# Kernel tuning notes

Measured on AMD Instinct MI355X. Metric: run time of the kernel, lower is better.

## Reference

```python
import jax, jax.numpy as jnp
import numpy as np

N = 100000
E = 3200000
IN_CH = 512
H1 = 16


def setup_inputs() -> dict:
    key = jax.random.key(0)
    ks = jax.random.split(key, 9)
    x = jax.random.normal(ks[0], (N, IN_CH), dtype=jnp.float32)
    edge_index = jax.random.randint(ks[1], (2, E), 0, N, dtype=jnp.int64)
    # GCNConv params: weight [in, out], bias [out]
    def glorot(k, fan_in, fan_out):
        lim = (6.0 / (fan_in + fan_out)) ** 0.5
        return jax.random.uniform(k, (fan_in, fan_out), jnp.float32, -lim, lim)
    W1 = glorot(ks[2], IN_CH, H1)
    b1 = jnp.zeros((H1,), jnp.float32)
    W2 = glorot(ks[3], H1, H1)
    b2 = jnp.zeros((H1,), jnp.float32)
    W3 = glorot(ks[4], H1, 1)
    b3 = jnp.zeros((1,), jnp.float32)
    return {"x": x, "edge_index": edge_index, "W1": W1, "b1": b1,
            "W2": W2, "b2": b2, "W3": W3, "b3": b3}


def _gcn_conv(x, W, b, src, dst, deg_isqrt):
    # GCNConv: h = X W; out = D^-1/2 (A + I) D^-1/2 h + b
    h = x @ W  # [N, out]
    norm = deg_isqrt[src] * deg_isqrt[dst]  # [E]
    msg = h[src] * norm[:, None]  # gather + scale
    agg = jax.ops.segment_sum(msg, dst, num_segments=N)  # scatter-add
    agg = agg + h * (deg_isqrt * deg_isqrt)[:, None]  # self-loop term
    return agg + b


def reference(x, edge_index, W1, b1, W2, b2, W3, b3):
    src, dst = edge_index[0], edge_index[1]
    # degree of A + I, counted on destination nodes (symmetric norm)
    deg = jax.ops.segment_sum(jnp.ones((E,), jnp.float32), dst, num_segments=N) + 1.0
    deg_isqrt = jax.lax.rsqrt(deg)
    h = _gcn_conv(x, W1, b1, src, dst, deg_isqrt)
    h = jax.nn.relu(h)  # dropout is identity at eval
    h = _gcn_conv(h, W2, b2, src, dst, deg_isqrt)
    h = jax.nn.relu(h)
    out = _gcn_conv(h, W3, b3, src, dst, deg_isqrt)
    return out
```

## Files before the change

kernel.cpp:

```cpp
#include <hip/hip_runtime.h>
#include <hip/hip_bf16.h>

static constexpr int N_NODES = 100000;
static constexpr int N_EDGES = 3200000;
static constexpr int IN_CH = 512;
static constexpr int H = 16;
static constexpr int TB = 256;

static constexpr int BN = 256;
static constexpr int NB = (N_NODES + BN - 1) / BN;
static constexpr int CAP = 8960;
static constexpr int CAP2 = CAP + 3 * BN;
static constexpr int CHUNK = 8192;
static constexpr int GRID_SC = (N_EDGES + CHUNK - 1) / CHUNK;
static constexpr int NBLK64 = (N_NODES + 63) / 64;

__global__ void k_init(int* __restrict__ gcur) {
  int b = blockIdx.x * blockDim.x + threadIdx.x;
  if (b < NB) gcur[b] = b * CAP;
}

__global__ void k_cscatter(const int* __restrict__ ei, int* __restrict__ gcur,
                           int* __restrict__ ebuf) {
  __shared__ int cnt[NB];
  __shared__ int gofs[NB];
  int t = threadIdx.x;
  int c0 = blockIdx.x * CHUNK;
  int c1 = min(c0 + CHUNK, N_EDGES);
  for (int b = t; b < NB; b += TB) cnt[b] = 0;
  __syncthreads();
  for (int j = c0 + t; j < c1; j += TB) atomicAdd(&cnt[ei[N_EDGES + j] >> 8], 1);
  __syncthreads();
  for (int b = t; b < NB; b += TB)
    if (cnt[b] > 0) gofs[b] = atomicAdd(&gcur[b], cnt[b]);
  __syncthreads();
  for (int j = c0 + t; j < c1; j += TB) {
    int s = ei[j];
    int d = ei[N_EDGES + j];
    int slot = atomicAdd(&gofs[d >> 8], 1);
    ebuf[slot] = ((d & 255) << 17) | s;
  }
}

__global__ void k_bsort(const int* __restrict__ gcur, const int* __restrict__ ebuf,
                        int* __restrict__ ebuf2, int* __restrict__ nrs,
                        int* __restrict__ nend, float* __restrict__ disq) {
  __shared__ int cnt[BN];
  __shared__ int pre[BN];
  __shared__ int cur[BN];
  int b = blockIdx.x, t = threadIdx.x;
  cnt[t] = 0;
  __syncthreads();
  int beg = b * CAP, end = gcur[b];
  for (int j = beg + t; j < end; j += TB) atomicAdd(&cnt[ebuf[j] >> 17], 1);
  __syncthreads();
  int myc = cnt[t];
  int ac = (myc + 3) & ~3;
  pre[t] = ac;
  __syncthreads();
  for (int off = 1; off < TB; off <<= 1) {
    int v = (t >= off) ? pre[t - off] : 0;
    __syncthreads();
    pre[t] += v;
    __syncthreads();
  }
  int start = b * CAP2 + ((t == 0) ? 0 : pre[t - 1]);
  cur[t] = start;
  int node = b * BN + t;
  if (node < N_NODES) {
    nrs[node] = start;
    nend[node] = start + ac;
    disq[node] = 1.0f / sqrtf((float)myc + 1.0f);
    for (int j = start + myc; j < start + ac; j++) ebuf2[j] = N_NODES;
  }
  __syncthreads();
  for (int j = beg + t; j < end; j += TB) {
    int p = ebuf[j];
    int slot = atomicAdd(&cur[p >> 17], 1);
    ebuf2[slot] = p & 0x1FFFF;
  }
}

__global__ void k_gemm1(const float* __restrict__ x, const float* __restrict__ W,
                        const float* __restrict__ disq,
                        float* __restrict__ hloA, float* __restrict__ hhiA,
                        float* __restrict__ hloB, float* __restrict__ hhiB,
                        float* __restrict__ hs3) {
  int r = blockIdx.x * blockDim.x + threadIdx.x;
  if (r > N_NODES) return;
  if (r == N_NODES) {
    float4 z = make_float4(0.f, 0.f, 0.f, 0.f);
    ((float4*)(hloA + (size_t)r * 8))[0] = z;
    ((float4*)(hloA + (size_t)r * 8))[1] = z;
    ((float4*)(hhiA + (size_t)r * 8))[0] = z;
    ((float4*)(hhiA + (size_t)r * 8))[1] = z;
    ((float4*)(hloB + (size_t)r * 8))[0] = z;
    ((float4*)(hloB + (size_t)r * 8))[1] = z;
    ((float4*)(hhiB + (size_t)r * 8))[0] = z;
    ((float4*)(hhiB + (size_t)r * 8))[1] = z;
    hs3[r] = 0.f;
    return;
  }
  const float4* xr = (const float4*)(x + (size_t)r * IN_CH);
  float acc[H];
#pragma unroll
  for (int c = 0; c < H; c++) acc[c] = 0.f;
  for (int k4 = 0; k4 < IN_CH / 4; k4++) {
    float4 xv = xr[k4];
    const float* wr = W + k4 * 4 * H;
    float xs[4] = {xv.x, xv.y, xv.z, xv.w};
#pragma unroll
    for (int j = 0; j < 4; j++) {
#pragma unroll
      for (int c = 0; c < H; c++) acc[c] = fmaf(xs[j], wr[j * H + c], acc[c]);
    }
  }
  float dn = disq[r];
  float4* lo = (float4*)(hloA + (size_t)r * 8);
  float4* hi = (float4*)(hhiA + (size_t)r * 8);
  lo[0] = make_float4(acc[0] * dn, acc[1] * dn, acc[2] * dn, acc[3] * dn);
  lo[1] = make_float4(acc[4] * dn, acc[5] * dn, acc[6] * dn, acc[7] * dn);
  hi[0] = make_float4(acc[8] * dn, acc[9] * dn, acc[10] * dn, acc[11] * dn);
  hi[1] = make_float4(acc[12] * dn, acc[13] * dn, acc[14] * dn, acc[15] * dn);
}

__global__ void k_gath_mid(const int* __restrict__ nrs, const int* __restrict__ nend,
                           const int* __restrict__ ebuf2, const float* __restrict__ disq,
                           const float* __restrict__ inlo, const float* __restrict__ inhi,
                           const float* __restrict__ W2, const float* __restrict__ bias,
                           float* __restrict__ outlo, float* __restrict__ outhi) {
  __shared__ float agg[64 * 16];
  __shared__ float w[256];
  int b = blockIdx.x, t = threadIdx.x;
  w[t] = W2[t];
  int grp = t >> 3, lane = t & 7;
#pragma unroll
  for (int ph = 0; ph < 2; ph++) {
    const float* hs = ph ? inhi : inlo;
#pragma unroll
    for (int k = 0; k < 2; k++) {
      int node = b * 64 + grp * 2 + k;
      if (node < N_NODES) {
        int beg = nrs[node], endp = nend[node];
        float acc = 0.f;
        for (int j = beg; j < endp; j += 4) {
          int4 s = *(const int4*)(ebuf2 + j);
          float a0 = hs[(size_t)s.x * 8 + lane];
          float a1 = hs[(size_t)s.y * 8 + lane];
          float a2 = hs[(size_t)s.z * 8 + lane];
          float a3 = hs[(size_t)s.w * 8 + lane];
          acc += (a0 + a1) + (a2 + a3);
        }
        float dn = disq[node];
        agg[(grp * 2 + k) * 16 + ph * 8 + lane] =
            fmaf(acc + hs[(size_t)node * 8 + lane], dn, bias[ph * 8 + lane]);
      }
    }
  }
  __syncthreads();
  int nl = t >> 2, q = t & 3;
  int node = b * 64 + nl;
  if (node < N_NODES) {
    float o0 = 0.f, o1 = 0.f, o2 = 0.f, o3 = 0.f;
#pragma unroll
    for (int c4 = 0; c4 < 4; c4++) {
      float4 av = *(const float4*)(agg + nl * 16 + c4 * 4);
      float vs[4] = {av.x, av.y, av.z, av.w};
#pragma unroll
      for (int i2 = 0; i2 < 4; i2++) {
        float v = fmaxf(vs[i2], 0.f);
        const float* wr = w + (c4 * 4 + i2) * 16 + q * 4;
        o0 = fmaf(v, wr[0], o0);
        o1 = fmaf(v, wr[1], o1);
        o2 = fmaf(v, wr[2], o2);
        o3 = fmaf(v, wr[3], o3);
      }
    }
    float dn = disq[node];
    float4 r = make_float4(o0 * dn, o1 * dn, o2 * dn, o3 * dn);
    if (q < 2) *(float4*)(outlo + (size_t)node * 8 + q * 4) = r;
    else *(float4*)(outhi + (size_t)node * 8 + (q - 2) * 4) = r;
  }
}

__global__ void k_gath_last(const int* __restrict__ nrs, const int* __restrict__ nend,
                            const int* __restrict__ ebuf2, const float* __restrict__ disq,
                            const float* __restrict__ inlo, const float* __restrict__ inhi,
                            const float* __restrict__ W3, const float* __restrict__ bias,
                            float* __restrict__ hs3) {
  __shared__ float agg[64 * 16];
  __shared__ float w3[16];
  int b = blockIdx.x, t = threadIdx.x;
  if (t < 16) w3[t] = W3[t];
  int grp = t >> 3, lane = t & 7;
#pragma unroll
  for (int ph = 0; ph < 2; ph++) {
    const float* hs = ph ? inhi : inlo;
#pragma unroll
    for (int k = 0; k < 2; k++) {
      int node = b * 64 + grp * 2 + k;
      if (node < N_NODES) {
        int beg = nrs[node], endp = nend[node];
        float acc = 0.f;
        for (int j = beg; j < endp; j += 4) {
          int4 s = *(const int4*)(ebuf2 + j);
          float a0 = hs[(size_t)s.x * 8 + lane];
          float a1 = hs[(size_t)s.y * 8 + lane];
          float a2 = hs[(size_t)s.z * 8 + lane];
          float a3 = hs[(size_t)s.w * 8 + lane];
          acc += (a0 + a1) + (a2 + a3);
        }
        float dn = disq[node];
        agg[(grp * 2 + k) * 16 + ph * 8 + lane] =
            fmaf(acc + hs[(size_t)node * 8 + lane], dn, bias[ph * 8 + lane]);
      }
    }
  }
  __syncthreads();
  int nl = t >> 2, q = t & 3;
  int node = b * 64 + nl;
  if (node < N_NODES) {
    float4 av = *(const float4*)(agg + nl * 16 + q * 4);
    float o = fmaxf(av.x, 0.f) * w3[q * 4 + 0];
    o = fmaf(fmaxf(av.y, 0.f), w3[q * 4 + 1], o);
    o = fmaf(fmaxf(av.z, 0.f), w3[q * 4 + 2], o);
    o = fmaf(fmaxf(av.w, 0.f), w3[q * 4 + 3], o);
    o += __shfl_xor(o, 1);
    o += __shfl_xor(o, 2);
    if (q == 0) hs3[node] = o * disq[node];
  }
}

__global__ void k_gath1(const int* __restrict__ nrs, const int* __restrict__ nend,
                        const int* __restrict__ ebuf2, const float* __restrict__ disq,
                        const float* __restrict__ hs3, const float* __restrict__ bias,
                        float* __restrict__ out) {
  int b = blockIdx.x, t = threadIdx.x;
  int nl = t >> 2, lane = t & 3;
  int node = b * 64 + nl;
  if (node >= N_NODES) return;
  int beg = nrs[node], endp = nend[node];
  float acc = 0.f;
  for (int j = beg + 4 * lane; j < endp; j += 16) {
    int4 s = *(const int4*)(ebuf2 + j);
    acc += (hs3[s.x] + hs3[s.y]) + (hs3[s.z] + hs3[s.w]);
  }
  acc += __shfl_xor(acc, 1);
  acc += __shfl_xor(acc, 2);
  if (lane == 0) out[node] = fmaf(acc + hs3[node], disq[node], bias[0]);
}

extern "C" void kernel_launch(void* const* d_in, const int* in_sizes, int n_in,
                              void* d_out, int out_size, void* d_ws, size_t ws_size,
                              hipStream_t stream) {
  const float* x = (const float*)d_in[0];
  const int* ei = (const int*)d_in[1];
  const float* W1 = (const float*)d_in[2];
  const float* b1 = (const float*)d_in[3];
  const float* W2 = (const float*)d_in[4];
  const float* b2 = (const float*)d_in[5];
  const float* W3 = (const float*)d_in[6];
  const float* b3 = (const float*)d_in[7];
  float* out = (float*)d_out;

  int* ebuf = (int*)d_ws;
  int* ebuf2 = ebuf + (size_t)NB * CAP;
  int* gcur = ebuf2 + (size_t)NB * CAP2;
  int* nrs = gcur + NB;
  int* nend = nrs + N_NODES;
  int pad = (4 - ((NB + 2 * N_NODES) & 3)) & 3;
  float* disq = (float*)(nend + N_NODES + pad);
  float* hloA = disq + N_NODES;
  float* hhiA = hloA + (size_t)(N_NODES + 1) * 8;
  float* hloB = hhiA + (size_t)(N_NODES + 1) * 8;
  float* hhiB = hloB + (size_t)(N_NODES + 1) * 8;
  float* hs3 = hhiB + (size_t)(N_NODES + 1) * 8;

  k_init<<<(NB + 63) / 64, 64, 0, stream>>>(gcur);
  k_cscatter<<<GRID_SC, TB, 0, stream>>>(ei, gcur, ebuf);
  k_bsort<<<NB, TB, 0, stream>>>(gcur, ebuf, ebuf2, nrs, nend, disq);

  k_gemm1<<<(N_NODES + 64) / 64, 64, 0, stream>>>(x, W1, disq, hloA, hhiA, hloB, hhiB, hs3);
  k_gath_mid<<<NBLK64, TB, 0, stream>>>(nrs, nend, ebuf2, disq, hloA, hhiA, W2, b1, hloB, hhiB);
  k_gath_last<<<NBLK64, TB, 0, stream>>>(nrs, nend, ebuf2, disq, hloB, hhiB, W3, b2, hs3);
  k_gath1<<<NBLK64, TB, 0, stream>>>(nrs, nend, ebuf2, disq, hs3, b3, out);
}
```

Measured before the change: 552.4 us.

## Store hidden features as contiguous 16-float rows and gather with float4 loads

Replaces the split lo/hi 8-float feature buffers with one 64-byte row per node. The gather kernels now use 4 lanes per node, each loading a float4, instead of 8 lanes doing scalar loads over two passes. The last layer's gather and W3 projection are fused into registers, which drops the shared-memory staging and a block sync. The aim is fewer, wider memory transactions per edge and fewer passes over the edge list, with one 64-byte line per neighbour instead of two 32-byte segments. In exchange each thread holds more loads in flight, and there are fewer threads per node.

```diff
diff --git a/kernel.cpp b/kernel.cpp
--- a/kernel.cpp
+++ b/kernel.cpp
@@ -83,21 +83,17 @@
 
 __global__ void k_gemm1(const float* __restrict__ x, const float* __restrict__ W,
                         const float* __restrict__ disq,
-                        float* __restrict__ hloA, float* __restrict__ hhiA,
-                        float* __restrict__ hloB, float* __restrict__ hhiB,
+                        float* __restrict__ hsA, float* __restrict__ hsB,
                         float* __restrict__ hs3) {
   int r = blockIdx.x * blockDim.x + threadIdx.x;
   if (r > N_NODES) return;
   if (r == N_NODES) {
     float4 z = make_float4(0.f, 0.f, 0.f, 0.f);
-    ((float4*)(hloA + (size_t)r * 8))[0] = z;
-    ((float4*)(hloA + (size_t)r * 8))[1] = z;
-    ((float4*)(hhiA + (size_t)r * 8))[0] = z;
-    ((float4*)(hhiA + (size_t)r * 8))[1] = z;
-    ((float4*)(hloB + (size_t)r * 8))[0] = z;
-    ((float4*)(hloB + (size_t)r * 8))[1] = z;
-    ((float4*)(hhiB + (size_t)r * 8))[0] = z;
-    ((float4*)(hhiB + (size_t)r * 8))[1] = z;
+#pragma unroll
+    for (int q = 0; q < 4; q++) {
+      ((float4*)(hsA + (size_t)r * H))[q] = z;
+      ((float4*)(hsB + (size_t)r * H))[q] = z;
+    }
     hs3[r] = 0.f;
     return;
   }
@@ -116,50 +112,51 @@
     }
   }
   float dn = disq[r];
-  float4* lo = (float4*)(hloA + (size_t)r * 8);
-  float4* hi = (float4*)(hhiA + (size_t)r * 8);
-  lo[0] = make_float4(acc[0] * dn, acc[1] * dn, acc[2] * dn, acc[3] * dn);
-  lo[1] = make_float4(acc[4] * dn, acc[5] * dn, acc[6] * dn, acc[7] * dn);
-  hi[0] = make_float4(acc[8] * dn, acc[9] * dn, acc[10] * dn, acc[11] * dn);
-  hi[1] = make_float4(acc[12] * dn, acc[13] * dn, acc[14] * dn, acc[15] * dn);
+  float4* o = (float4*)(hsA + (size_t)r * H);
+#pragma unroll
+  for (int q = 0; q < 4; q++)
+    o[q] = make_float4(acc[4 * q + 0] * dn, acc[4 * q + 1] * dn,
+                       acc[4 * q + 2] * dn, acc[4 * q + 3] * dn);
 }
 
 __global__ void k_gath_mid(const int* __restrict__ nrs, const int* __restrict__ nend,
                            const int* __restrict__ ebuf2, const float* __restrict__ disq,
-                           const float* __restrict__ inlo, const float* __restrict__ inhi,
-                           const float* __restrict__ W2, const float* __restrict__ bias,
-                           float* __restrict__ outlo, float* __restrict__ outhi) {
+                           const float* __restrict__ hs, const float* __restrict__ W2,
+                           const float* __restrict__ bias, float* __restrict__ ouths) {
   __shared__ float agg[64 * 16];
   __shared__ float w[256];
   int b = blockIdx.x, t = threadIdx.x;
   w[t] = W2[t];
-  int grp = t >> 3, lane = t & 7;
-#pragma unroll
-  for (int ph = 0; ph < 2; ph++) {
-    const float* hs = ph ? inhi : inlo;
-#pragma unroll
-    for (int k = 0; k < 2; k++) {
-      int node = b * 64 + grp * 2 + k;
-      if (node < N_NODES) {
-        int beg = nrs[node], endp = nend[node];
-        float acc = 0.f;
-        for (int j = beg; j < endp; j += 4) {
-          int4 s = *(const int4*)(ebuf2 + j);
-          float a0 = hs[(size_t)s.x * 8 + lane];
-          float a1 = hs[(size_t)s.y * 8 + lane];
-          float a2 = hs[(size_t)s.z * 8 + lane];
-          float a3 = hs[(size_t)s.w * 8 + lane];
-          acc += (a0 + a1) + (a2 + a3);
-        }
-        float dn = disq[node];
-        agg[(grp * 2 + k) * 16 + ph * 8 + lane] =
-            fmaf(acc + hs[(size_t)node * 8 + lane], dn, bias[ph * 8 + lane]);
-      }
-    }
+  int grp = t >> 2, lane = t & 3;
+  int node = b * 64 + grp;
+  const float4* hs4 = (const float4*)hs;
+  if (node < N_NODES) {
+    int beg = nrs[node], endp = nend[node];
+    float4 a = make_float4(0.f, 0.f, 0.f, 0.f);
+    for (int j = beg; j < endp; j += 4) {
+      int4 s = *(const int4*)(ebuf2 + j);
+      float4 v0 = hs4[s.x * 4 + lane];
+      float4 v1 = hs4[s.y * 4 + lane];
+      float4 v2 = hs4[s.z * 4 + lane];
+      float4 v3 = hs4[s.w * 4 + lane];
+      a.x += (v0.x + v1.x) + (v2.x + v3.x);
+      a.y += (v0.y + v1.y) + (v2.y + v3.y);
+      a.z += (v0.z + v1.z) + (v2.z + v3.z);
+      a.w += (v0.w + v1.w) + (v2.w + v3.w);
+    }
+    float dn = disq[node];
+    float4 self = hs4[node * 4 + lane];
+    float4 bv = *(const float4*)(bias + lane * 4);
+    float4 r;
+    r.x = fmaf(a.x + self.x, dn, bv.x);
+    r.y = fmaf(a.y + self.y, dn, bv.y);
+    r.z = fmaf(a.z + self.z, dn, bv.z);
+    r.w = fmaf(a.w + self.w, dn, bv.w);
+    *(float4*)(agg + grp * 16 + lane * 4) = r;
   }
   __syncthreads();
   int nl = t >> 2, q = t & 3;
-  int node = b * 64 + nl;
+  node = b * 64 + nl;
   if (node < N_NODES) {
     float o0 = 0.f, o1 = 0.f, o2 = 0.f, o3 = 0.f;
 #pragma unroll
@@ -177,58 +174,49 @@
       }
     }
     float dn = disq[node];
-    float4 r = make_float4(o0 * dn, o1 * dn, o2 * dn, o3 * dn);
-    if (q < 2) *(float4*)(outlo + (size_t)node * 8 + q * 4) = r;
-    else *(float4*)(outhi + (size_t)node * 8 + (q - 2) * 4) = r;
+    *(float4*)(ouths + (size_t)node * H + q * 4) =
+        make_float4(o0 * dn, o1 * dn, o2 * dn, o3 * dn);
   }
 }
 
 __global__ void k_gath_last(const int* __restrict__ nrs, const int* __restrict__ nend,
                             const int* __restrict__ ebuf2, const float* __restrict__ disq,
-                            const float* __restrict__ inlo, const float* __restrict__ inhi,
-                            const float* __restrict__ W3, const float* __restrict__ bias,
-                            float* __restrict__ hs3) {
-  __shared__ float agg[64 * 16];
-  __shared__ float w3[16];
-  int b = blockIdx.x, t = threadIdx.x;
-  if (t < 16) w3[t] = W3[t];
-  int grp = t >> 3, lane = t & 7;
-#pragma unroll
-  for (int ph = 0; ph < 2; ph++) {
-    const float* hs = ph ? inhi : inlo;
-#pragma unroll
-    for (int k = 0; k < 2; k++) {
-      int node = b * 64 + grp * 2 + k;
-      if (node < N_NODES) {
-        int beg = nrs[node], endp = nend[node];
-        float acc = 0.f;
-        for (int j = beg; j < endp; j += 4) {
-          int4 s = *(const int4*)(ebuf2 + j);
-          float a0 = hs[(size_t)s.x * 8 + lane];
-          float a1 = hs[(size_t)s.y * 8 + lane];
-          float a2 = hs[(size_t)s.z * 8 + lane];
-          float a3 = hs[(size_t)s.w * 8 + lane];
-          acc += (a0 + a1) + (a2 + a3);
-        }
-        float dn = disq[node];
-        agg[(grp * 2 + k) * 16 + ph * 8 + lane] =
-            fmaf(acc + hs[(size_t)node * 8 + lane], dn, bias[ph * 8 + lane]);
-      }
-    }
-  }
-  __syncthreads();
-  int nl = t >> 2, q = t & 3;
-  int node = b * 64 + nl;
-  if (node < N_NODES) {
-    float4 av = *(const float4*)(agg + nl * 16 + q * 4);
-    float o = fmaxf(av.x, 0.f) * w3[q * 4 + 0];
-    o = fmaf(fmaxf(av.y, 0.f), w3[q * 4 + 1], o);
-    o = fmaf(fmaxf(av.z, 0.f), w3[q * 4 + 2], o);
-    o = fmaf(fmaxf(av.w, 0.f), w3[q * 4 + 3], o);
-    o += __shfl_xor(o, 1);
-    o += __shfl_xor(o, 2);
-    if (q == 0) hs3[node] = o * disq[node];
-  }
+                            const float* __restrict__ hs, const float* __restrict__ W3,
+                            const float* __restrict__ bias, float* __restrict__ hs3) {
+  int b = blockIdx.x, t = threadIdx.x;
+  int grp = t >> 2, lane = t & 3;
+  int node = b * 64 + grp;
+  if (node >= N_NODES) return;
+  const float4* hs4 = (const float4*)hs;
+  int beg = nrs[node], endp = nend[node];
+  float4 a = make_float4(0.f, 0.f, 0.f, 0.f);
+  for (int j = beg; j < endp; j += 4) {
+    int4 s = *(const int4*)(ebuf2 + j);
+    float4 v0 = hs4[s.x * 4 + lane];
+    float4 v1 = hs4[s.y * 4 + lane];
+    float4 v2 = hs4[s.z * 4 + lane];
+    float4 v3 = hs4[s.w * 4 + lane];
+    a.x += (v0.x + v1.x) + (v2.x + v3.x);
+    a.y += (v0.y + v1.y) + (v2.y + v3.y);
+    a.z += (v0.z + v1.z) + (v2.z + v3.z);
+    a.w += (v0.w + v1.w) + (v2.w + v3.w);
+  }
+  float dn = disq[node];
+  float4 self = hs4[node * 4 + lane];
+  float4 bv = *(const float4*)(bias + lane * 4);
+  float4 r;
+  r.x = fmaf(a.x + self.x, dn, bv.x);
+  r.y = fmaf(a.y + self.y, dn, bv.y);
+  r.z = fmaf(a.z + self.z, dn, bv.z);
+  r.w = fmaf(a.w + self.w, dn, bv.w);
+  const float4 wv = *(const float4*)(W3 + lane * 4);
+  float o = fmaxf(r.x, 0.f) * wv.x;
+  o = fmaf(fmaxf(r.y, 0.f), wv.y, o);
+  o = fmaf(fmaxf(r.z, 0.f), wv.z, o);
+  o = fmaf(fmaxf(r.w, 0.f), wv.w, o);
+  o += __shfl_xor(o, 1);
+  o += __shfl_xor(o, 2);
+  if (lane == 0) hs3[node] = o * dn;
 }
 
 __global__ void k_gath1(const int* __restrict__ nrs, const int* __restrict__ nend,
@@ -270,18 +258,16 @@
   int* nend = nrs + N_NODES;
   int pad = (4 - ((NB + 2 * N_NODES) & 3)) & 3;
   float* disq = (float*)(nend + N_NODES + pad);
-  float* hloA = disq + N_NODES;
-  float* hhiA = hloA + (size_t)(N_NODES + 1) * 8;
-  float* hloB = hhiA + (size_t)(N_NODES + 1) * 8;
-  float* hhiB = hloB + (size_t)(N_NODES + 1) * 8;
-  float* hs3 = hhiB + (size_t)(N_NODES + 1) * 8;
+  float* hsA = disq + N_NODES;
+  float* hsB = hsA + (size_t)(N_NODES + 1) * H;
+  float* hs3 = hsB + (size_t)(N_NODES + 1) * H;
 
   k_init<<<(NB + 63) / 64, 64, 0, stream>>>(gcur);
   k_cscatter<<<GRID_SC, TB, 0, stream>>>(ei, gcur, ebuf);
   k_bsort<<<NB, TB, 0, stream>>>(gcur, ebuf, ebuf2, nrs, nend, disq);
 
-  k_gemm1<<<(N_NODES + 64) / 64, 64, 0, stream>>>(x, W1, disq, hloA, hhiA, hloB, hhiB, hs3);
-  k_gath_mid<<<NBLK64, TB, 0, stream>>>(nrs, nend, ebuf2, disq, hloA, hhiA, W2, b1, hloB, hhiB);
-  k_gath_last<<<NBLK64, TB, 0, stream>>>(nrs, nend, ebuf2, disq, hloB, hhiB, W3, b2, hs3);
+  k_gemm1<<<(N_NODES + 64) / 64, 64, 0, stream>>>(x, W1, disq, hsA, hsB, hs3);
+  k_gath_mid<<<NBLK64, TB, 0, stream>>>(nrs, nend, ebuf2, disq, hsA, W2, b1, hsB);
+  k_gath_last<<<NBLK64, TB, 0, stream>>>(nrs, nend, ebuf2, disq, hsB, W3, b2, hs3);
   k_gath1<<<NBLK64, TB, 0, stream>>>(nrs, nend, ebuf2, disq, hs3, b3, out);
 }
```

Result: no change. 559.4 us (+1.3%).
